# Kernel tuning notes

Hardware: AMD Instinct MI355X
Metric: run time of the kernel (lower is better)

The kernel has to match this reference:

```python
import jax, jax.numpy as jnp
import numpy as np

B, T, D, K = 4, 4096, 256, 16


def hankel_eigvecs(T: int, k: int) -> jnp.ndarray:
    """Top-k |eigenvalue| eigenvectors of Z_ij = 2/((i+j)^3 - (i+j)), 1-indexed."""
    idx = np.arange(1, T + 1, dtype=np.float64)
    ij = idx[None, :] + idx[:, None]
    Z = 2.0 / (ij ** 3 - ij)
    w, v = np.linalg.eigh(Z)
    top = np.argsort(-np.abs(w))[:k]
    return jnp.asarray(v[:, top], dtype=jnp.float32)  # (T, K)


def setup_inputs() -> dict:
    key = jax.random.key(0)
    kx, kw = jax.random.split(key)
    x = jax.random.normal(kx, (B, T, D), dtype=jnp.float32)
    # Stacked weights of the K independent nn.Linear(D, D, bias=False) modules.
    # W[k] is the torch Linear weight (out, in); y = c @ W[k].T.
    W = jax.random.normal(kw, (K, D, D), dtype=jnp.float32) * (1.0 / np.sqrt(D))
    phi = hankel_eigvecs(T, K)  # Hankel eigenvector buffer (non-trainable)
    return {"x": x, "W": W, "phi": phi}


def reference(x, W, phi):
    # x: (B,T,D), W: (K,D,D), phi: (T,K)
    # c_k[t] = cumsum_{s<=t} phi[s,k] * x[s]   -> batched over all K filters
    C = jnp.cumsum(phi[None, :, :, None] * x[:, :, None, :], axis=1)  # (B,T,K,D)
    # out[t] = sum_k phi[t,k] * (c_k[t] @ W_k^T)
    out = jnp.einsum('btkd,ked,tk->bte', C, W, phi)  # (B,T,D)
    return out  # dropout is identity in eval mode (dropout=0.0)
```

## Files before the change

kernel.cpp:

```cpp
#include <hip/hip_runtime.h>


typedef __bf16 bf16x8 __attribute__((ext_vector_type(8)));
typedef float  f32x4  __attribute__((ext_vector_type(4)));
typedef unsigned short u16;

__device__ static inline u16 f2bf(float f) {
    unsigned int u = __float_as_uint(f);
    u = (u + 0x7fffu + ((u >> 16) & 1u)) >> 16;
    return (u16)u;
}

__device__ static inline void gload16(const void* g, void* l) {
    __builtin_amdgcn_global_load_lds((const __attribute__((address_space(1))) void*)g,
                                     (__attribute__((address_space(3))) void*)l, 16, 0, 0);
}

__global__ __launch_bounds__(256) void k0_wt(const float* __restrict__ W, u16* __restrict__ WT) {
    const int e = blockIdx.x, d = threadIdx.x;
    union { u16 u[16]; uint4 v[2]; } ob;
#pragma unroll
    for (int k = 0; k < 16; ++k)
        ob.u[k] = f2bf(W[((size_t)k * 256 + e) * 256 + d]);
    uint4* dst = (uint4*)(WT + (size_t)e * 4096 + d * 16);
    dst[0] = ob.v[0]; dst[1] = ob.v[1];
}

__global__ __launch_bounds__(256) void k1_sums(const float* __restrict__ x,
                                               const float* __restrict__ phi,
                                               float* __restrict__ U) {
    __shared__ float phis[256];
    const int tid = threadIdx.x;
    const int b = blockIdx.x, c = blockIdx.y;
    const int t0 = c * 16;
    phis[tid] = phi[t0 * 16 + tid];
    __syncthreads();
    float acc[16];
#pragma unroll
    for (int k = 0; k < 16; ++k) acc[k] = 0.f;
    for (int s = 0; s < 16; ++s) {
        const float xv = x[(size_t)((b << 12) + t0 + s) * 256 + tid];
        union { float f[16]; float4 v[4]; } pv;
#pragma unroll
        for (int j = 0; j < 4; ++j) pv.v[j] = *(const float4*)&phis[s * 16 + j * 4];
#pragma unroll
        for (int k = 0; k < 16; ++k) acc[k] = fmaf(pv.f[k], xv, acc[k]);
    }
    float4* Up = (float4*)(U + ((size_t)((b * 256 + c) * 256 + tid)) * 16);
    union { float f[16]; float4 v[4]; } ov;
#pragma unroll
    for (int k = 0; k < 16; ++k) ov.f[k] = acc[k];
#pragma unroll
    for (int j = 0; j < 4; ++j) Up[j] = ov.v[j];
}

__global__ __launch_bounds__(64) void k2_scan(float* __restrict__ U) {
    const int b = blockIdx.x;
    const int dk = blockIdx.y * 64 + threadIdx.x;
    float* base = U + (size_t)b * 1048576 + dk;
    float runv = 0.f;
    for (int g = 0; g < 16; ++g) {
        float v[16];
#pragma unroll
        for (int j = 0; j < 16; ++j) v[j] = base[(size_t)(g * 16 + j) * 4096];
#pragma unroll
        for (int j = 0; j < 16; ++j) {
            const float t = v[j];
            base[(size_t)(g * 16 + j) * 4096] = runv;
            runv += t;
        }
    }
}

__global__ __launch_bounds__(512, 4) void k4_fused(const float* __restrict__ x,
                                                   const float* __restrict__ phi,
                                                   const float* __restrict__ U,
                                                   const u16* __restrict__ BT,
                                                   float* __restrict__ C) {
    __shared__ __align__(16) char smem[81920];
    const int tid = threadIdx.x;
    const int m0 = blockIdx.x * 64;
    const int ks = blockIdx.y;
    const int b  = m0 >> 12, t0 = m0 & 4095, c0 = t0 >> 4;
    const int w = tid >> 6, l = tid & 63;
    const int wm = (w >> 2) * 32, wn = (w & 3) * 64;
    const int lg = l >> 4, lr = l & 15;
    f32x4 acc[2][4] = {};

    const int ch = w & 3, khi = w >> 2;
    const int klo = l & 7, dl = (l >> 3) & 3, sh = l >> 5;
    const int kl = khi * 8 + klo;
    const int row0 = ch * 16 + sh * 8;
    const int colb = (dl * 16 + kl) * 2;

    float p[8];
#pragma unroll
    for (int s = 0; s < 8; ++s) p[s] = phi[(t0 + row0 + s) * 16 + kl];

    const char* Bb = (const char*)BT;
    float xr[8], useed;

    auto bload = [&](int kt) {
        const int d = ks * 128 + kt * 4 + dl;
        const float* xp = x + (size_t)(m0 + row0) * 256 + d;
#pragma unroll
        for (int s = 0; s < 8; ++s) xr[s] = xp[(size_t)s * 256];
        useed = U[(((size_t)(b * 256 + c0 + ch)) * 256 + d) * 16 + kl];
    };
    auto stageB = [&](int kt, int buf) {
        const int kofs = ks * 4096 + kt * 128;
#pragma unroll
        for (int c = 0; c < 4; ++c) {
            const int row = c * 64 + (tid >> 3);
            gload16(Bb + (size_t)row * 8192 + kofs + (((tid & 7) * 16) ^ ((row & 7) << 4)),
                    smem + 16384 + buf * 32768 + c * 8192 + tid * 16);
        }
    };
    auto bcomp = [&](int buf) {
        float run = sh ? 0.f : useed;
        float ap[8];
#pragma unroll
        for (int s = 0; s < 8; ++s) { run = fmaf(p[s], xr[s], run); ap[s] = run; }
        const float cross = __shfl_xor(run, 32, 64);
        const float base = sh ? cross : 0.f;
        char* Ab = smem + buf * 8192 + row0 * 128;
#pragma unroll
        for (int s = 0; s < 8; ++s)
            *(__bf16*)(Ab + s * 128 + (colb ^ (s << 4))) = (__bf16)(p[s] * (ap[s] + base));
    };
    auto mfma_phase = [&](int buf) {
        const char* Abase = smem + buf * 8192;
        const char* Bbase = smem + 16384 + buf * 32768;
#pragma unroll
        for (int kk = 0; kk < 2; ++kk) {
            const int kb = kk * 64 + lg * 16;
            bf16x8 af[2], bfv[4];
#pragma unroll
            for (int mi = 0; mi < 2; ++mi) {
                const int r = wm + mi * 16 + lr;
                af[mi] = *(const bf16x8*)(Abase + r * 128 + (kb ^ ((r & 7) << 4)));
            }
#pragma unroll
            for (int ni = 0; ni < 4; ++ni) {
                const int n = wn + ni * 16 + lr;
                bfv[ni] = *(const bf16x8*)(Bbase + n * 128 + (kb ^ ((n & 7) << 4)));
            }
#pragma unroll
            for (int mi = 0; mi < 2; ++mi)
#pragma unroll
                for (int ni = 0; ni < 4; ++ni)
                    acc[mi][ni] = __builtin_amdgcn_mfma_f32_16x16x32_bf16(af[mi], bfv[ni], acc[mi][ni], 0, 0, 0);
        }
    };

    bload(0); stageB(0, 0); bcomp(0);
    __syncthreads();

    for (int kt = 0; kt < 32; ++kt) {
        const int cur = kt & 1;
        if (kt < 31) {
            bload(kt + 1);
            stageB(kt + 1, cur ^ 1);
        }
        mfma_phase(cur);
        if (kt < 31) bcomp(cur ^ 1);
        __syncthreads();
    }

#pragma unroll
    for (int mi = 0; mi < 2; ++mi)
#pragma unroll
        for (int ni = 0; ni < 4; ++ni)
#pragma unroll
            for (int r = 0; r < 4; ++r) {
                const int row = m0 + wm + mi * 16 + lg * 4 + r;
                const int col = wn + ni * 16 + lr;
                unsafeAtomicAdd(&C[(size_t)row * 256 + col], acc[mi][ni][r]);
            }
}

extern "C" void kernel_launch(void* const* d_in, const int* in_sizes, int n_in,
                              void* d_out, int out_size, void* d_ws, size_t ws_size,
                              hipStream_t stream) {
    const float* x   = (const float*)d_in[0];
    const float* W   = (const float*)d_in[1];
    const float* phi = (const float*)d_in[2];
    float* out = (float*)d_out;

    char* ws = (char*)d_ws;
    u16*   WT = (u16*)ws;
    float* U  = (float*)(ws + (2u << 20));

    k0_wt  <<<256, 256, 0, stream>>>(W, WT);
    k1_sums<<<dim3(4, 256), 256, 0, stream>>>(x, phi, U);
    k2_scan<<<dim3(4, 64), 64, 0, stream>>>(U);
    hipMemsetAsync(d_out, 0, (size_t)out_size * sizeof(float), stream);
    k4_fused<<<dim3(256, 2), 512, 0, stream>>>(x, phi, U, WT, out);
}
```

Before: 103.0 us.

## Single-buffer LDS, register-prefetch B, async-stage x/U, split K four ways

```diff
diff --git a/kernel.cpp b/kernel.cpp
--- a/kernel.cpp
+++ b/kernel.cpp
@@ -72,12 +72,12 @@
     }
 }
 
-__global__ __launch_bounds__(512, 4) void k4_fused(const float* __restrict__ x,
+__global__ __launch_bounds__(512, 6) void k4_fused(const float* __restrict__ x,
                                                    const float* __restrict__ phi,
                                                    const float* __restrict__ U,
                                                    const u16* __restrict__ BT,
                                                    float* __restrict__ C) {
-    __shared__ __align__(16) char smem[81920];
+    __shared__ __align__(16) char smem[45056];
     const int tid = threadIdx.x;
     const int m0 = blockIdx.x * 64;
     const int ks = blockIdx.y;
@@ -97,40 +97,56 @@
 #pragma unroll
     for (int s = 0; s < 8; ++s) p[s] = phi[(t0 + row0 + s) * 16 + kl];
 
-    const char* Bb = (const char*)BT;
-    float xr[8], useed;
-
-    auto bload = [&](int kt) {
-        const int d = ks * 128 + kt * 4 + dl;
-        const float* xp = x + (size_t)(m0 + row0) * 256 + d;
-#pragma unroll
-        for (int s = 0; s < 8; ++s) xr[s] = xp[(size_t)s * 256];
-        useed = U[(((size_t)(b * 256 + c0 + ch)) * 256 + d) * 16 + kl];
-    };
-    auto stageB = [&](int kt, int buf) {
-        const int kofs = ks * 4096 + kt * 128;
-#pragma unroll
-        for (int c = 0; c < 4; ++c) {
-            const int row = c * 64 + (tid >> 3);
-            gload16(Bb + (size_t)row * 8192 + kofs + (((tid & 7) * 16) ^ ((row & 7) << 4)),
-                    smem + 16384 + buf * 32768 + c * 8192 + tid * 16);
-        }
-    };
-    auto bcomp = [&](int buf) {
+    const int tr = tid >> 3;
+    const char* bsrc0 = (const char*)BT + (size_t)tr * 8192 + ks * 2048
+                        + (((tid & 7) * 16) ^ ((tr & 7) << 4));
+    const int bdst0 = 8192 + tid * 16;
+
+    const int sig = ((l & 7) << 3) | (l >> 3);
+    const char* xu_src;
+    if (w == 0)      xu_src = (const char*)x + ((size_t)(m0 + sig)) * 1024 + ks * 256;
+    else             xu_src = (const char*)U + ((size_t)(b * 256 + c0 + (l >> 4))) * 16384
+                              + ks * 4096 + ((l >> 2) & 3) * 64 + (l & 3) * 16;
+    const int xu_dst = (w == 0 ? 40960 : 43008) + l * 16;
+
+    auto stage_xu = [&](int kt, int slot) {
+        if (w == 0)      gload16(xu_src + kt * 16,  smem + xu_dst + slot * 1024);
+        else if (w == 1) gload16(xu_src + kt * 256, smem + xu_dst + slot * 1024);
+    };
+    uint4 br0, br1, br2, br3;
+    auto breg_load = [&](int kt) {
+        br0 = *(const uint4*)(bsrc0 + kt * 128);
+        br1 = *(const uint4*)(bsrc0 + 524288 + kt * 128);
+        br2 = *(const uint4*)(bsrc0 + 1048576 + kt * 128);
+        br3 = *(const uint4*)(bsrc0 + 1572864 + kt * 128);
+    };
+    auto bwrite = [&]() {
+        *(uint4*)(smem + bdst0)         = br0;
+        *(uint4*)(smem + bdst0 + 8192)  = br1;
+        *(uint4*)(smem + bdst0 + 16384) = br2;
+        *(uint4*)(smem + bdst0 + 24576) = br3;
+    };
+    auto bcomp = [&](int kt) {
+        const char* xb = smem + 40960 + (kt & 1) * 1024;
+        const char* ub = smem + 43008 + (kt & 1) * 1024;
+        const float useed = *(const float*)(ub + ch * 256 + dl * 64 + kl * 4);
         float run = sh ? 0.f : useed;
         float ap[8];
 #pragma unroll
-        for (int s = 0; s < 8; ++s) { run = fmaf(p[s], xr[s], run); ap[s] = run; }
+        for (int s = 0; s < 8; ++s) {
+            const float xv = *(const float*)(xb + ((s << 3) | (ch * 2 + sh)) * 16 + dl * 4);
+            run = fmaf(p[s], xv, run); ap[s] = run;
+        }
         const float cross = __shfl_xor(run, 32, 64);
         const float base = sh ? cross : 0.f;
-        char* Ab = smem + buf * 8192 + row0 * 128;
+        char* Ab = smem + row0 * 128;
 #pragma unroll
         for (int s = 0; s < 8; ++s)
             *(__bf16*)(Ab + s * 128 + (colb ^ (s << 4))) = (__bf16)(p[s] * (ap[s] + base));
     };
-    auto mfma_phase = [&](int buf) {
-        const char* Abase = smem + buf * 8192;
-        const char* Bbase = smem + 16384 + buf * 32768;
+    auto mfma_phase = [&]() {
+        const char* Abase = smem;
+        const char* Bbase = smem + 8192;
 #pragma unroll
         for (int kk = 0; kk < 2; ++kk) {
             const int kb = kk * 64 + lg * 16;
@@ -153,18 +169,24 @@
         }
     };
 
-    bload(0); stageB(0, 0); bcomp(0);
+    breg_load(0);
+    stage_xu(0, 0);
+    stage_xu(1, 1);
     __syncthreads();
-
-    for (int kt = 0; kt < 32; ++kt) {
-        const int cur = kt & 1;
-        if (kt < 31) {
-            bload(kt + 1);
-            stageB(kt + 1, cur ^ 1);
-        }
-        mfma_phase(cur);
-        if (kt < 31) bcomp(cur ^ 1);
+    bwrite();
+    bcomp(0);
+    __syncthreads();
+
+    for (int kt = 0; kt < 16; ++kt) {
+        if (kt < 15) breg_load(kt + 1);
+        if (kt < 14) stage_xu(kt + 2, kt & 1);
+        mfma_phase();
         __syncthreads();
+        if (kt < 15) {
+            bwrite();
+            bcomp(kt + 1);
+            __syncthreads();
+        }
     }
 
 #pragma unroll
@@ -195,5 +217,5 @@
     k1_sums<<<dim3(4, 256), 256, 0, stream>>>(x, phi, U);
     k2_scan<<<dim3(4, 64), 64, 0, stream>>>(U);
     hipMemsetAsync(d_out, 0, (size_t)out_size * sizeof(float), stream);
-    k4_fused<<<dim3(256, 2), 512, 0, stream>>>(x, phi, U, WT, out);
-}
+    k4_fused<<<dim3(256, 4), 512, 0, stream>>>(x, phi, U, WT, out);
+}
```

Result: slower. 220.6 us (+114.3%).
